# Optimization experiments

Hardware: AMD Instinct MI355X
Metric: run time of the kernel (lower is better)

Reference implementation:

```python
import jax, jax.numpy as jnp
import numpy as np

KNN = 32

def _sqdist(src, dst):
    # src [B,N,C], dst [B,M,C] -> [B,N,M]
    return (jnp.sum(src * src, -1)[:, :, None]
            + jnp.sum(dst * dst, -1)[:, None, :]
            - 2.0 * jnp.einsum('bnc,bmc->bnm', src, dst))

def _knn(points, queries, k):
    d = _sqdist(queries, points)
    neg_d, idx = jax.lax.top_k(-d, k)  # smallest-k, sorted ascending
    return -neg_d, idx

def _gather(points, idx):
    # points [B,N,C], idx [B,S,K] -> [B,S,K,C]
    return jax.vmap(lambda p, i: p[i])(points, idx)

def _bn(x, gamma, beta):
    # BatchNorm1d over channel dim, stats over (B, N), training-mode (biased var)
    mean = jnp.mean(x, axis=(0, 1), keepdims=True)
    var = jnp.var(x, axis=(0, 1), keepdims=True)
    return gamma * (x - mean) * jax.lax.rsqrt(var + 1e-5) + beta

def _lin_bn_act(x, W, b, gamma, beta):
    return jax.nn.leaky_relu(_bn(x @ W + b, gamma, beta), 0.2)

def _local_trans(feat, idx, qW, qb, kW, kb, vW, vb, rW, rb, rg, rbe, fW, fb, fg, fbe):
    # xyz=False, FPS_idx=None, usetanh=False branch of LocalTrans
    residual = _lin_bn_act(feat, rW, rb, rg, rbe)          # conv_res (residual=True)
    q = (feat @ qW + qb)[:, :, None, :]                    # [B,N,1,C]
    k = _gather(feat @ kW + kb, idx)                       # [B,N,K,C]
    v = _gather(feat @ vW + vb, idx)                       # [B,N,K,C]
    energy = (q - k) / jnp.sqrt(jnp.float32(qW.shape[-1]))
    att = jax.nn.softmax(energy, axis=2)                   # softmax over K
    att = att - jnp.sum(att, axis=2, keepdims=True)        # offset subtraction
    ctx = jnp.max(att * v, axis=2)                         # max-pool over K -> [B,N,C]
    return residual + _lin_bn_act(ctx, fW, fb, fg, fbe)    # ffn


def setup_inputs() -> dict:
    key = jax.random.key(0)
    ks = jax.random.split(key, 12)
    B, N, Cin, Cout = 4, 2048, 128, 256
    r = lambda k, s: jax.random.normal(k, s, dtype=jnp.float32)
    return {
        'xyz': r(ks[0], (B, N, 3)),
        'base_xyz': r(ks[1], (B, N, 3)),
        'feature': r(ks[2], (B, N, Cin)),
        'qW': r(ks[3], (2, Cin, Cout)) * 0.05, 'qb': jnp.zeros((2, Cout), jnp.float32),
        'kW': r(ks[4], (2, Cin, Cout)) * 0.05, 'kb': jnp.zeros((2, Cout), jnp.float32),
        'vW': r(ks[5], (2, Cin, Cout)) * 0.05, 'vb': jnp.zeros((2, Cout), jnp.float32),
        'resW': r(ks[6], (2, Cin, Cout)) * 0.05, 'resb': jnp.zeros((2, Cout), jnp.float32),
        'res_gamma': jnp.ones((2, Cout), jnp.float32), 'res_beta': jnp.zeros((2, Cout), jnp.float32),
        'ffnW': r(ks[7], (2, Cout, Cout)) * 0.05, 'ffnb': jnp.zeros((2, Cout), jnp.float32),
        'ffn_gamma': jnp.ones((2, Cout), jnp.float32), 'ffn_beta': jnp.zeros((2, Cout), jnp.float32),
        'fcW': r(ks[8], (2 * Cout, Cout)) * 0.05, 'fcb': jnp.zeros((Cout,), jnp.float32),
        'fc_gamma': jnp.ones((Cout,), jnp.float32), 'fc_beta': jnp.zeros((Cout,), jnp.float32),
    }


def reference(xyz, base_xyz, feature, qW, qb, kW, kb, vW, vb, resW, resb,
              res_gamma, res_beta, ffnW, ffnb, ffn_gamma, ffn_beta,
              fcW, fcb, fc_gamma, fc_beta):
    # LocalMerge.forward, branch: feature is not None, FPS_idx is None
    dist, idx = _knn(base_xyz, xyz, KNN)
    _, idx_feature = _knn(feature, feature, KNN)
    idxs = (idx, idx_feature)
    ms = [_local_trans(feature, idxs[i], qW[i], qb[i], kW[i], kb[i], vW[i], vb[i],
                       resW[i], resb[i], res_gamma[i], res_beta[i],
                       ffnW[i], ffnb[i], ffn_gamma[i], ffn_beta[i]) for i in range(2)]
    merge = _lin_bn_act(jnp.concatenate(ms, axis=2), fcW, fcb, fc_gamma, fc_beta)
    return merge
```

## Files before the change

kernel.cpp:

```cpp
#include <hip/hip_runtime.h>
#include <hip/hip_bf16.h>

typedef __hip_bfloat16 bf16;
typedef __attribute__((ext_vector_type(8))) short short8;
typedef __attribute__((ext_vector_type(4))) float f32x4;

#define ROWS 8192
#define NPTS 2048
#define CIN  128
#define COUT 256
#define KNN  32
#define PAD  132

__device__ inline float lrelu(float x){ return x >= 0.f ? x : 0.2f*x; }
__device__ inline unsigned short f2bf(float x){
  bf16 h = __float2bfloat16(x);
  return *(unsigned short*)&h;
}
__device__ inline float bf2f(unsigned short u){ return __uint_as_float((unsigned)u << 16); }
__device__ inline void stc(float* p, float v){ *p = v; }
__device__ inline void stc(unsigned short* p, float v){ *p = f2bf(v); }

#define N_WTX   (2048*CIN)
#define N_WFFN  (2*COUT*COUT)
#define N_WFC   (COUT*512)
#define N_FEAT  (ROWS*CIN)
__global__ __launch_bounds__(256) void pack_all(
    const float* qW, const float* kW, const float* vW, const float* rW,
    const float* qb, const float* kb, const float* vb, const float* rb,
    const float* ffnW, const float* fcW, const float* feature,
    unsigned short* WT_x, float* bcat, unsigned short* WT_ffn,
    unsigned short* WT_fc, unsigned short* feat_bf){
  int t = blockIdx.x*256 + threadIdx.x;
  if (t < N_WTX){
    int c = t >> 7, r = t & 127;
    int g = c >> 8, i = g >> 2, tt = g & 3, cc = c & 255;
    const float* W = (tt==0?qW: tt==1?kW: tt==2?vW: rW) + (size_t)i*CIN*COUT;
    WT_x[t] = f2bf(W[r*COUT + cc]);
    if (r == 0){
      const float* bb = (tt==0?qb: tt==1?kb: tt==2?vb: rb) + i*COUT;
      bcat[c] = bb[cc];
    }
  } else if (t < N_WTX + N_WFFN){
    int u = t - N_WTX;
    int i = u >> 16, n = (u >> 8) & 255, k = u & 255;
    WT_ffn[u] = f2bf(ffnW[(size_t)i*65536 + k*256 + n]);
  } else if (t < N_WTX + N_WFFN + N_WFC){
    int u = t - N_WTX - N_WFFN;
    int n = u >> 9, k = u & 511;
    WT_fc[u] = f2bf(fcW[(size_t)k*256 + n]);
  } else {
    int u = t - N_WTX - N_WFFN - N_WFC;
    feat_bf[u] = f2bf(feature[u]);
  }
}

__device__ inline unsigned dxf(float d){
  unsigned u = __float_as_uint(d);
  return (u & 0x80000000u) ? ~u : (u | 0x80000000u);
}
__device__ inline unsigned umin32(unsigned a, unsigned b){ return a < b ? a : b; }

#define DPP_ROW_SHR1    0x111
#define DPP_ROW_SHR2    0x112
#define DPP_ROW_SHR4    0x114
#define DPP_ROW_SHR8    0x118

template<int CTRL>
__device__ inline unsigned dpp_umin_step(unsigned v){
  unsigned s = (unsigned)__builtin_amdgcn_update_dpp((int)v, (int)v, CTRL, 0xF, 0xF, false);
  return s < v ? s : v;
}

#define TOPK32_CASE(G)                                                   \
  {                                                                      \
    int jw = 7;                                                          \
    _Pragma("unroll")                                                    \
    for (int j = 7; j >= 0; --j) if (k[G*8+j] == minv) jw = j;           \
    slot = G*8 + jw;                                                     \
    _Pragma("unroll")                                                    \
    for (int j = 0; j < 8; ++j) if (j == jw) k[G*8+j] = ~0u;             \
    unsigned nm = k[G*8];                                                \
    _Pragma("unroll")                                                    \
    for (int j = 1; j < 8; ++j) nm = umin32(nm, k[G*8+j]);               \
    g[G] = nm;                                                           \
  }

__device__ inline void wave_topk32_u32(unsigned* k, int lane, int* out){
  unsigned g[4];
  #pragma unroll
  for (int gi = 0; gi < 4; ++gi){
    unsigned m = k[gi*8];
    #pragma unroll
    for (int j = 1; j < 8; ++j) m = umin32(m, k[gi*8+j]);
    g[gi] = m;
  }
  unsigned outv = 0;
  for (int r = 0; r < KNN; ++r){
    unsigned lm = umin32(umin32(g[0], g[1]), umin32(g[2], g[3]));
    unsigned m = lm;
    m = dpp_umin_step<DPP_ROW_SHR1>(m);
    m = dpp_umin_step<DPP_ROW_SHR2>(m);
    m = dpp_umin_step<DPP_ROW_SHR4>(m);
    m = dpp_umin_step<DPP_ROW_SHR8>(m);
    unsigned b0 = (unsigned)__builtin_amdgcn_readlane((int)m, 15);
    unsigned b1 = (unsigned)__builtin_amdgcn_readlane((int)m, 31);
    unsigned b2 = (unsigned)__builtin_amdgcn_readlane((int)m, 47);
    unsigned b3 = (unsigned)__builtin_amdgcn_readlane((int)m, 63);
    unsigned minv = umin32(umin32(b0, b1), umin32(b2, b3));
    unsigned long long ball = __ballot(lm == minv);
    int owner = (int)__builtin_ctzll(ball);
    int slot = 0;
    if (owner == lane){
      int gw = (g[0]==minv) ? 0 : (g[1]==minv) ? 1 : (g[2]==minv) ? 2 : 3;
      if      (gw == 0) TOPK32_CASE(0)
      else if (gw == 1) TOPK32_CASE(1)
      else if (gw == 2) TOPK32_CASE(2)
      else              TOPK32_CASE(3)
    }
    int slotw = __builtin_amdgcn_readlane(slot, owner);
    unsigned wm = (unsigned)(owner*32 + slotw);
    outv = (lane == r) ? wm : outv;
  }
  if (lane < KNN) out[lane] = (int)outv;
}

__device__ inline unsigned dkey_xyz(float qq, float q0, float q1, float q2,
                                    float p0, float p1, float p2){
  float pp = __fadd_rn(__fadd_rn(__fmul_rn(p0,p0), __fmul_rn(p1,p1)), __fmul_rn(p2,p2));
  float dot = __fmul_rn(q0,p0);
  dot = __fadd_rn(dot, __fmul_rn(q1,p1));
  dot = __fadd_rn(dot, __fmul_rn(q2,p2));
  float d = __fsub_rn(__fadd_rn(qq, pp), __fmul_rn(2.f, dot));
  return dxf(d);
}

__global__ __launch_bounds__(256, 6) void knn_xyz_kernel(const float* xyz, const float* base, int* idx_out){
  int wave = threadIdx.x >> 6;
  int lane = threadIdx.x & 63;
  int bid = blockIdx.x*4 + wave;
  int b = bid >> 11;
  float q0 = xyz[(size_t)bid*3+0];
  float q1 = xyz[(size_t)bid*3+1];
  float q2 = xyz[(size_t)bid*3+2];
  float qq = __fadd_rn(__fadd_rn(__fmul_rn(q0,q0), __fmul_rn(q1,q1)), __fmul_rn(q2,q2));
  const float4* p4 = (const float4*)(base + (size_t)b*NPTS*3 + (size_t)lane*96);
  unsigned k[32];
  #pragma unroll
  for (int c = 0; c < 8; ++c){
    float4 f0 = p4[c*3+0];
    float4 f1 = p4[c*3+1];
    float4 f2 = p4[c*3+2];
    k[c*4+0] = dkey_xyz(qq,q0,q1,q2, f0.x, f0.y, f0.z);
    k[c*4+1] = dkey_xyz(qq,q0,q1,q2, f0.w, f1.x, f1.y);
    k[c*4+2] = dkey_xyz(qq,q0,q1,q2, f1.z, f1.w, f2.x);
    k[c*4+3] = dkey_xyz(qq,q0,q1,q2, f2.y, f2.z, f2.w);
  }
  wave_topk32_u32(k, lane, idx_out + (size_t)bid*KNN);
}

__global__ __launch_bounds__(256) void rownorm_kernel(const float* feat, float* nrm){
  int row = blockIdx.x*256 + threadIdx.x;
  const float* f = feat + (size_t)row*CIN;
  float L[16];
  #pragma unroll
  for (int l = 0; l < 16; ++l){
    float x0 = __fmul_rn(f[l],     f[l]);
    float x1 = __fmul_rn(f[16+l],  f[16+l]);
    float x2 = __fmul_rn(f[32+l],  f[32+l]);
    float x3 = __fmul_rn(f[48+l],  f[48+l]);
    float x4 = __fmul_rn(f[64+l],  f[64+l]);
    float x5 = __fmul_rn(f[80+l],  f[80+l]);
    float x6 = __fmul_rn(f[96+l],  f[96+l]);
    float x7 = __fmul_rn(f[112+l], f[112+l]);
    L[l] = __fadd_rn(
        __fadd_rn(__fadd_rn(x0,x1), __fadd_rn(x2,x3)),
        __fadd_rn(__fadd_rn(x4,x5), __fadd_rn(x6,x7)));
  }
  float T2[4];
  #pragma unroll
  for (int i = 0; i < 4; ++i)
    T2[i] = __fadd_rn(__fadd_rn(L[i], L[i+8]), __fadd_rn(L[i+4], L[i+12]));
  nrm[row] = __fadd_rn(__fadd_rn(T2[0], T2[2]), __fadd_rn(T2[1], T2[3]));
}

__global__ __launch_bounds__(256) void dist_feat_kernel(const float* fb, const float* nrm, float* D){
  __shared__ float Aq[32*PAD];
  __shared__ float Bm[32*PAD];
  int nb = blockIdx.y*32, mb = blockIdx.x*32;
  int t = threadIdx.x;
  {
    int r = t >> 3, c16 = (t & 7) << 4;
    const float* an = fb + (size_t)(nb + r)*CIN + c16;
    const float* bm = fb + (size_t)(mb + r)*CIN + c16;
    #pragma unroll
    for (int j = 0; j < 4; ++j){
      *(float4*)&Aq[r*PAD + c16 + 4*j] = *(const float4*)&an[4*j];
      *(float4*)&Bm[r*PAD + c16 + 4*j] = *(const float4*)&bm[4*j];
    }
  }
  __syncthreads();
  int tx = t & 15, ty = t >> 4;
  const float* qa0 = &Aq[(ty     )*PAD];
  const float* qa1 = &Aq[(ty + 16)*PAD];
  const float* ma0 = &Bm[(tx     )*PAD];
  const float* ma1 = &Bm[(tx + 16)*PAD];
  float P[2][2][16];
  #pragma unroll
  for (int l = 0; l < 16; ++l){
    float a0 = qa0[48+l], a1 = qa1[48+l], b0 = ma0[48+l], b1 = ma1[48+l];
    P[0][0][l] = __fmul_rn(a0,b0); P[0][1][l] = __fmul_rn(a0,b1);
    P[1][0][l] = __fmul_rn(a1,b0); P[1][1][l] = __fmul_rn(a1,b1);
  }
  const int segs[7] = {32,16,0,112,96,80,64};
  #pragma unroll
  for (int s = 0; s < 7; ++s){
    int off = segs[s];
    #pragma unroll
    for (int l = 0; l < 16; ++l){
      float a0 = qa0[off+l], a1 = qa1[off+l], b0 = ma0[off+l], b1 = ma1[off+l];
      P[0][0][l] = __fmaf_rn(a0,b0,P[0][0][l]); P[0][1][l] = __fmaf_rn(a0,b1,P[0][1][l]);
      P[1][0][l] = __fmaf_rn(a1,b0,P[1][0][l]); P[1][1][l] = __fmaf_rn(a1,b1,P[1][1][l]);
    }
  }
  #pragma unroll
  for (int i = 0; i < 2; ++i){
    int n = nb + ty + 16*i;
    float nn = nrm[n];
    #pragma unroll
    for (int j = 0; j < 2; ++j){
      float T2[4];
      #pragma unroll
      for (int q = 0; q < 4; ++q)
        T2[q] = __fadd_rn(__fadd_rn(P[i][j][q], P[i][j][q+8]), __fadd_rn(P[i][j][q+4], P[i][j][q+12]));
      float dot = __fadd_rn(__fadd_rn(T2[0], T2[2]), __fadd_rn(T2[1], T2[3]));
      int m = mb + tx + 16*j;
      D[(size_t)n*NPTS + m] = __fsub_rn(__fadd_rn(nn, nrm[m]), __fmul_rn(2.f, dot));
    }
  }
}

__global__ __launch_bounds__(256, 6) void topk_row_kernel(const float* D, int* idx_out){
  int wave = threadIdx.x >> 6;
  int lane = threadIdx.x & 63;
  int n = blockIdx.x*4 + wave;
  const float* src = D + (size_t)n*NPTS + lane*32;
  unsigned k[32];
  #pragma unroll
  for (int i = 0; i < 8; ++i){
    float4 v = *(const float4*)&src[i*4];
    k[i*4+0] = dxf(v.x);
    k[i*4+1] = dxf(v.y);
    k[i*4+2] = dxf(v.z);
    k[i*4+3] = dxf(v.w);
  }
  wave_topk32_u32(k, lane, idx_out + (size_t)n*KNN);
}

template<typename CT>
__global__ __launch_bounds__(256) void mfma_gemm(const unsigned short* __restrict__ A,
                                                 const unsigned short* __restrict__ Bt,
                                                 const float* __restrict__ bias,
                                                 CT* __restrict__ C, int N, int K,
                                                 size_t sA, size_t sB, size_t sBias, size_t sC){
  int z = blockIdx.z;
  A += (size_t)z*sA; Bt += (size_t)z*sB; bias += (size_t)z*sBias; C += (size_t)z*sC;
  __shared__ unsigned short As[64*40];
  __shared__ unsigned short Bs[64*40];
  int nb = blockIdx.x*64, mb = blockIdx.y*64;
  int t = threadIdx.x;
  int wave = t >> 6, lane = t & 63;
  int m16 = lane & 15, quad = lane >> 4;
  f32x4 acc[4];
  #pragma unroll
  for (int s = 0; s < 4; ++s) acc[s] = (f32x4){0.f, 0.f, 0.f, 0.f};
  int srow = t >> 2, skseg = (t & 3) << 3;
  for (int kt = 0; kt < K; kt += 32){
    __syncthreads();
    *(uint4*)&As[srow*40 + skseg] = *(const uint4*)&A [(size_t)(mb + srow)*K + kt + skseg];
    *(uint4*)&Bs[srow*40 + skseg] = *(const uint4*)&Bt[(size_t)(nb + srow)*K + kt + skseg];
    __syncthreads();
    short8 a = *(const short8*)&As[(wave*16 + m16)*40 + quad*8];
    #pragma unroll
    for (int s = 0; s < 4; ++s){
      short8 b = *(const short8*)&Bs[(s*16 + m16)*40 + quad*8];
      acc[s] = __builtin_amdgcn_mfma_f32_16x16x32_bf16(a, b, acc[s], 0, 0, 0);
    }
  }
  #pragma unroll
  for (int s = 0; s < 4; ++s){
    int col = nb + s*16 + m16;
    float bv = bias[col];
    #pragma unroll
    for (int r = 0; r < 4; ++r){
      int row = mb + wave*16 + quad*4 + r;
      stc(&C[(size_t)row*N + col], acc[s][r] + bv);
    }
  }
}

__global__ __launch_bounds__(256) void attn_kernel(const unsigned short* X,
                                                   const int* idx0, const int* idx1,
                                                   unsigned short* ctx){
  int i = blockIdx.y;
  const int* ip = (i == 0 ? idx0 : idx1);
  int local = threadIdx.x & 127;
  int r     = threadIdx.x >> 7;
  int bn    = blockIdx.x*2 + r;
  int b     = bn >> 11;
  __shared__ int jr[2][KNN];
  if (local < KNN) jr[r][local] = (b << 11) + ip[(size_t)bn*KNN + local];
  __syncthreads();
  const ushort2* X2 = (const ushort2*)X;
  size_t boff = (size_t)i*512 + local;
  ushort2 q2 = X2[(size_t)bn*1024 + boff];
  float qx = bf2f(q2.x), qy = bf2f(q2.y);
  float ex[KNN], ey[KNN];
  float mx = -3.4e38f, my = -3.4e38f;
  #pragma unroll
  for (int k = 0; k < KNN; ++k){
    ushort2 k2 = X2[(size_t)jr[r][k]*1024 + boff + 128];
    ex[k] = (qx - bf2f(k2.x)) * 0.0625f;
    ey[k] = (qy - bf2f(k2.y)) * 0.0625f;
    mx = fmaxf(mx, ex[k]);
    my = fmaxf(my, ey[k]);
  }
  float sx = 0.f, sy = 0.f;
  #pragma unroll
  for (int k = 0; k < KNN; ++k){
    sx += __expf(ex[k] - mx);
    sy += __expf(ey[k] - my);
  }
  float ix = 1.f / sx, iy = 1.f / sy;
  float bx = -3.4e38f, by = -3.4e38f;
  #pragma unroll
  for (int k = 0; k < KNN; ++k){
    ushort2 v2 = X2[(size_t)jr[r][k]*1024 + boff + 256];
    float ax = __expf(ex[k] - mx)*ix - 1.0f;
    float ay = __expf(ey[k] - my)*iy - 1.0f;
    bx = fmaxf(bx, ax*bf2f(v2.x));
    by = fmaxf(by, ay*bf2f(v2.y));
  }
  ushort2 o; o.x = f2bf(bx); o.y = f2bf(by);
  ((ushort2*)ctx)[((size_t)i*ROWS + bn)*128 + local] = o;
}

__global__ __launch_bounds__(256) void bnx_partial(const unsigned short* X, float* partial){
  int p = blockIdx.x, i = blockIdx.y, c = threadIdx.x;
  const unsigned short* base = X + (size_t)i*1024 + 768 + c;
  float s = 0.f, s2 = 0.f;
  for (int r = 0; r < 256; ++r){
    float v = bf2f(base[(size_t)(p*256 + r)*2048]);
    s += v; s2 += v*v;
  }
  partial[((size_t)i*32 + p)*512 + c]       = s;
  partial[((size_t)i*32 + p)*512 + 256 + c] = s2;
}

__global__ __launch_bounds__(256) void bnf_partial(const unsigned short* F, float* partial){
  int p = blockIdx.x, i = blockIdx.y, c = threadIdx.x;
  const unsigned short* base = F + (size_t)i*ROWS*COUT + c;
  float s = 0.f, s2 = 0.f;
  for (int r = 0; r < 256; ++r){
    float v = bf2f(base[(size_t)(p*256 + r)*COUT]);
    s += v; s2 += v*v;
  }
  partial[((size_t)i*32 + p)*512 + c]       = s;
  partial[((size_t)i*32 + p)*512 + 256 + c] = s2;
}

__global__ __launch_bounds__(256) void bny_partial(const float* Y, float* partial){
  int p = blockIdx.x, c = threadIdx.x;
  float s = 0.f, s2 = 0.f;
  for (int r = 0; r < 256; ++r){
    float v = Y[(size_t)(p*256 + r)*COUT + c];
    s += v; s2 += v*v;
  }
  partial[p*512 + c]       = s;
  partial[p*512 + 256 + c] = s2;
}

__global__ __launch_bounds__(256) void bn_final2(const float* partial, float* stats){
  int i = blockIdx.y, c = threadIdx.x;
  partial += (size_t)i*32*512;
  stats   += (size_t)i*512;
  float s = 0.f, s2 = 0.f;
  for (int p = 0; p < 32; ++p){ s += partial[p*512 + c]; s2 += partial[p*512 + 256 + c]; }
  float mean = s * (1.f/8192.f);
  float var  = s2 * (1.f/8192.f) - mean*mean;
  stats[c]       = mean;
  stats[256 + c] = 1.f / sqrtf(var + 1e-5f);
}

__global__ __launch_bounds__(256) void build_m_kernel(const unsigned short* X, const unsigned short* F,
    const float* stats, const float* gR, const float* bR, const float* gF, const float* bF,
    unsigned short* M){
  int bn = blockIdx.x, c = threadIdx.x;
  #pragma unroll
  for (int i = 0; i < 2; ++i){
    float r  = bf2f(X[(size_t)bn*2048 + i*1024 + 768 + c]);
    float rv = gR[i*COUT+c] * (r - stats[i*512+c]) * stats[i*512+256+c] + bR[i*COUT+c];
    rv = lrelu(rv);
    float f  = bf2f(F[(size_t)i*ROWS*COUT + (size_t)bn*COUT + c]);
    float fv = gF[i*COUT+c] * (f - stats[(2+i)*512+c]) * stats[(2+i)*512+256+c] + bF[i*COUT+c];
    fv = lrelu(fv);
    M[(size_t)bn*512 + i*COUT + c] = f2bf(rv + fv);
  }
}

__global__ __launch_bounds__(256) void final_kernel(const float* Y, const float* stats,
                                                    const float* g, const float* be, float* out){
  int bn = blockIdx.x, c = threadIdx.x;
  float y = Y[(size_t)bn*COUT + c];
  float v = g[c] * (y - stats[c]) * stats[256+c] + be[c];
  out[(size_t)bn*COUT + c] = lrelu(v);
}

extern "C" void kernel_launch(void* const* d_in, const int* in_sizes, int n_in,
                              void* d_out, int out_size, void* d_ws, size_t ws_size,
                              hipStream_t stream){
  const float* xyz      = (const float*)d_in[0];
  const float* base_xyz = (const float*)d_in[1];
  const float* feature  = (const float*)d_in[2];
  const float* qW = (const float*)d_in[3];
  const float* qb = (const float*)d_in[4];
  const float* kW = (const float*)d_in[5];
  const float* kb = (const float*)d_in[6];
  const float* vW = (const float*)d_in[7];
  const float* vb = (const float*)d_in[8];
  const float* rW = (const float*)d_in[9];
  const float* rb = (const float*)d_in[10];
  const float* res_gamma = (const float*)d_in[11];
  const float* res_beta  = (const float*)d_in[12];
  const float* ffnW = (const float*)d_in[13];
  const float* ffnb = (const float*)d_in[14];
  const float* ffn_gamma = (const float*)d_in[15];
  const float* ffn_beta  = (const float*)d_in[16];
  const float* fcW = (const float*)d_in[17];
  const float* fcb = (const float*)d_in[18];
  const float* fc_gamma = (const float*)d_in[19];
  const float* fc_beta  = (const float*)d_in[20];
  float* out = (float*)d_out;

  char* ws = (char*)d_ws;
  size_t o = 0;
  auto alloc = [&](size_t bytes)->char*{
    char* p = ws + o;
    o += (bytes + 255) & ~(size_t)255;
    return p;
  };
  int*            idx0    = (int*)           alloc((size_t)ROWS*KNN*4);
  int*            idx1    = (int*)           alloc((size_t)ROWS*KNN*4);
  float*          nrm     = (float*)         alloc((size_t)ROWS*4);
  float*          bcat    = (float*)         alloc((size_t)2048*4);
  unsigned short* WT_x    = (unsigned short*)alloc((size_t)2048*CIN*2);
  unsigned short* WT_ffn  = (unsigned short*)alloc((size_t)2*COUT*COUT*2);
  unsigned short* WT_fc   = (unsigned short*)alloc((size_t)COUT*512*2);
  unsigned short* feat_bf = (unsigned short*)alloc((size_t)ROWS*CIN*2);
  float*          stats   = (float*)         alloc((size_t)5*512*4);
  float*          partial = (float*)         alloc((size_t)2*32*512*4);
  char*           R1      = alloc((size_t)ROWS*2048*2);
  char*           R2      = alloc((size_t)ROWS*COUT*4);
  unsigned short* Mmat_bf = (unsigned short*)alloc((size_t)ROWS*512*2);
  unsigned short* F_bf    = (unsigned short*)alloc((size_t)2*ROWS*COUT*2);
  float*          Dbuf = (float*)R1;
  unsigned short* X_bf = (unsigned short*)R1;
  unsigned short* ctx_bf = (unsigned short*)R2;
  float*          Y    = (float*)R2;

  pack_all<<<(N_WTX+N_WFFN+N_WFC+N_FEAT)/256, 256, 0, stream>>>(
      qW,kW,vW,rW,qb,kb,vb,rb, ffnW, fcW, feature, WT_x, bcat, WT_ffn, WT_fc, feat_bf);

  knn_xyz_kernel<<<ROWS/4, 256, 0, stream>>>(xyz, base_xyz, idx0);
  rownorm_kernel<<<ROWS/256, 256, 0, stream>>>(feature, nrm);

  for (int b = 0; b < 4; ++b){
    const float* fb = feature + (size_t)b*NPTS*CIN;
    dist_feat_kernel<<<dim3(NPTS/32, NPTS/32), 256, 0, stream>>>(
        fb, nrm + (size_t)b*NPTS, Dbuf);
    topk_row_kernel<<<NPTS/4, 256, 0, stream>>>(Dbuf, idx1 + (size_t)b*NPTS*KNN);
  }

  mfma_gemm<unsigned short><<<dim3(2048/64, ROWS/64, 1), 256, 0, stream>>>(
      feat_bf, WT_x, bcat, X_bf, 2048, CIN, 0, 0, 0, 0);

  attn_kernel<<<dim3(ROWS/2, 2), 256, 0, stream>>>(X_bf, idx0, idx1, ctx_bf);

  bnx_partial<<<dim3(32, 2), 256, 0, stream>>>(X_bf, partial);
  bn_final2<<<dim3(1, 2), 256, 0, stream>>>(partial, stats);

  mfma_gemm<unsigned short><<<dim3(COUT/64, ROWS/64, 2), 256, 0, stream>>>(
      ctx_bf, WT_ffn, ffnb, F_bf, COUT, COUT,
      (size_t)ROWS*COUT, (size_t)COUT*COUT, COUT, (size_t)ROWS*COUT);

  bnf_partial<<<dim3(32, 2), 256, 0, stream>>>(F_bf, partial);
  bn_final2<<<dim3(1, 2), 256, 0, stream>>>(partial, stats + 2*512);

  build_m_kernel<<<ROWS, 256, 0, stream>>>(X_bf, F_bf, stats,
      res_gamma, res_beta, ffn_gamma, ffn_beta, Mmat_bf);

  mfma_gemm<float><<<dim3(COUT/64, ROWS/64, 1), 256, 0, stream>>>(
      Mmat_bf, WT_fc, fcb, Y, COUT, 512, 0, 0, 0, 0);

  bny_partial<<<32, 256, 0, stream>>>(Y, partial);
  bn_final2<<<dim3(1, 1), 256, 0, stream>>>(partial, stats + 4*512);

  final_kernel<<<ROWS, 256, 0, stream>>>(Y, stats + 4*512, fc_gamma, fc_beta, out);
}
```

Baseline: 471.8 us.

## Exploit distance symmetry, precompute base point norms, cache softmax exponentials

The feature self-distance kernel now computes only the upper-triangular tiles and writes each tile's transpose through shared memory, roughly halving the FMA work. The base_xyz squared norms are precomputed once in the packing kernel instead of being recomputed by every query wave in the xyz kNN. The attention kernel keeps its exponentials in registers instead of computing them twice. The risks are higher register pressure in attention, an extra shared-memory transpose pass, and uneven block work in the distance kernel.

```diff
diff --git a/kernel.cpp b/kernel.cpp
--- a/kernel.cpp
+++ b/kernel.cpp
@@ -25,12 +25,13 @@
 #define N_WFFN  (2*COUT*COUT)
 #define N_WFC   (COUT*512)
 #define N_FEAT  (ROWS*CIN)
+#define N_PP    8192
 __global__ __launch_bounds__(256) void pack_all(
     const float* qW, const float* kW, const float* vW, const float* rW,
     const float* qb, const float* kb, const float* vb, const float* rb,
-    const float* ffnW, const float* fcW, const float* feature,
+    const float* ffnW, const float* fcW, const float* feature, const float* base_xyz,
     unsigned short* WT_x, float* bcat, unsigned short* WT_ffn,
-    unsigned short* WT_fc, unsigned short* feat_bf){
+    unsigned short* WT_fc, unsigned short* feat_bf, float* ppxyz){
   int t = blockIdx.x*256 + threadIdx.x;
   if (t < N_WTX){
     int c = t >> 7, r = t & 127;
@@ -49,9 +50,15 @@
     int u = t - N_WTX - N_WFFN;
     int n = u >> 9, k = u & 511;
     WT_fc[u] = f2bf(fcW[(size_t)k*256 + n]);
-  } else {
+  } else if (t < N_WTX + N_WFFN + N_WFC + N_FEAT){
     int u = t - N_WTX - N_WFFN - N_WFC;
     feat_bf[u] = f2bf(feature[u]);
+  } else {
+    int u = t - N_WTX - N_WFFN - N_WFC - N_FEAT;
+    float p0 = base_xyz[(size_t)u*3+0];
+    float p1 = base_xyz[(size_t)u*3+1];
+    float p2 = base_xyz[(size_t)u*3+2];
+    ppxyz[u] = __fadd_rn(__fadd_rn(__fmul_rn(p0,p0), __fmul_rn(p1,p1)), __fmul_rn(p2,p2));
   }
 }
 
@@ -126,8 +133,7 @@
 }
 
 __device__ inline unsigned dkey_xyz(float qq, float q0, float q1, float q2,
-                                    float p0, float p1, float p2){
-  float pp = __fadd_rn(__fadd_rn(__fmul_rn(p0,p0), __fmul_rn(p1,p1)), __fmul_rn(p2,p2));
+                                    float p0, float p1, float p2, float pp){
   float dot = __fmul_rn(q0,p0);
   dot = __fadd_rn(dot, __fmul_rn(q1,p1));
   dot = __fadd_rn(dot, __fmul_rn(q2,p2));
@@ -135,7 +141,8 @@
   return dxf(d);
 }
 
-__global__ __launch_bounds__(256, 6) void knn_xyz_kernel(const float* xyz, const float* base, int* idx_out){
+__global__ __launch_bounds__(256, 6) void knn_xyz_kernel(const float* xyz, const float* base,
+                                                         const float* ppxyz, int* idx_out){
   int wave = threadIdx.x >> 6;
   int lane = threadIdx.x & 63;
   int bid = blockIdx.x*4 + wave;
@@ -145,16 +152,18 @@
   float q2 = xyz[(size_t)bid*3+2];
   float qq = __fadd_rn(__fadd_rn(__fmul_rn(q0,q0), __fmul_rn(q1,q1)), __fmul_rn(q2,q2));
   const float4* p4 = (const float4*)(base + (size_t)b*NPTS*3 + (size_t)lane*96);
+  const float4* n4 = (const float4*)(ppxyz + (size_t)b*NPTS + (size_t)lane*32);
   unsigned k[32];
   #pragma unroll
   for (int c = 0; c < 8; ++c){
     float4 f0 = p4[c*3+0];
     float4 f1 = p4[c*3+1];
     float4 f2 = p4[c*3+2];
-    k[c*4+0] = dkey_xyz(qq,q0,q1,q2, f0.x, f0.y, f0.z);
-    k[c*4+1] = dkey_xyz(qq,q0,q1,q2, f0.w, f1.x, f1.y);
-    k[c*4+2] = dkey_xyz(qq,q0,q1,q2, f1.z, f1.w, f2.x);
-    k[c*4+3] = dkey_xyz(qq,q0,q1,q2, f2.y, f2.z, f2.w);
+    float4 pn = n4[c];
+    k[c*4+0] = dkey_xyz(qq,q0,q1,q2, f0.x, f0.y, f0.z, pn.x);
+    k[c*4+1] = dkey_xyz(qq,q0,q1,q2, f0.w, f1.x, f1.y, pn.y);
+    k[c*4+2] = dkey_xyz(qq,q0,q1,q2, f1.z, f1.w, f2.x, pn.z);
+    k[c*4+3] = dkey_xyz(qq,q0,q1,q2, f2.y, f2.z, f2.w, pn.w);
   }
   wave_topk32_u32(k, lane, idx_out + (size_t)bid*KNN);
 }
@@ -188,6 +197,7 @@
   __shared__ float Aq[32*PAD];
   __shared__ float Bm[32*PAD];
   int nb = blockIdx.y*32, mb = blockIdx.x*32;
+  if (mb < nb) return;
   int t = threadIdx.x;
   {
     int r = t >> 3, c16 = (t & 7) << 4;
@@ -223,6 +233,7 @@
       P[1][0][l] = __fmaf_rn(a1,b0,P[1][0][l]); P[1][1][l] = __fmaf_rn(a1,b1,P[1][1][l]);
     }
   }
+  float val[2][2];
   #pragma unroll
   for (int i = 0; i < 2; ++i){
     int n = nb + ty + 16*i;
@@ -235,9 +246,24 @@
         T2[q] = __fadd_rn(__fadd_rn(P[i][j][q], P[i][j][q+8]), __fadd_rn(P[i][j][q+4], P[i][j][q+12]));
       float dot = __fadd_rn(__fadd_rn(T2[0], T2[2]), __fadd_rn(T2[1], T2[3]));
       int m = mb + tx + 16*j;
-      D[(size_t)n*NPTS + m] = __fsub_rn(__fadd_rn(nn, nrm[m]), __fmul_rn(2.f, dot));
-    }
-  }
+      float v = __fsub_rn(__fadd_rn(nn, nrm[m]), __fmul_rn(2.f, dot));
+      val[i][j] = v;
+      D[(size_t)n*NPTS + m] = v;
+    }
+  }
+  __syncthreads();
+  float* Tt = Aq;
+  #pragma unroll
+  for (int i = 0; i < 2; ++i)
+    #pragma unroll
+    for (int j = 0; j < 2; ++j)
+      Tt[(tx + 16*j)*33 + (ty + 16*i)] = val[i][j];
+  __syncthreads();
+  #pragma unroll
+  for (int i = 0; i < 2; ++i)
+    #pragma unroll
+    for (int j = 0; j < 2; ++j)
+      D[(size_t)(mb + ty + 16*i)*NPTS + (nb + tx + 16*j)] = Tt[(ty + 16*i)*33 + (tx + 16*j)];
 }
 
 __global__ __launch_bounds__(256, 6) void topk_row_kernel(const float* D, int* idx_out){
@@ -328,16 +354,18 @@
   float sx = 0.f, sy = 0.f;
   #pragma unroll
   for (int k = 0; k < KNN; ++k){
-    sx += __expf(ex[k] - mx);
-    sy += __expf(ey[k] - my);
+    ex[k] = __expf(ex[k] - mx);
+    ey[k] = __expf(ey[k] - my);
+    sx += ex[k];
+    sy += ey[k];
   }
   float ix = 1.f / sx, iy = 1.f / sy;
   float bx = -3.4e38f, by = -3.4e38f;
   #pragma unroll
   for (int k = 0; k < KNN; ++k){
     ushort2 v2 = X2[(size_t)jr[r][k]*1024 + boff + 256];
-    float ax = __expf(ex[k] - mx)*ix - 1.0f;
-    float ay = __expf(ey[k] - my)*iy - 1.0f;
+    float ax = ex[k]*ix - 1.0f;
+    float ay = ey[k]*iy - 1.0f;
     bx = fmaxf(bx, ax*bf2f(v2.x));
     by = fmaxf(by, ay*bf2f(v2.y));
   }
@@ -452,6 +480,7 @@
   int*            idx0    = (int*)           alloc((size_t)ROWS*KNN*4);
   int*            idx1    = (int*)           alloc((size_t)ROWS*KNN*4);
   float*          nrm     = (float*)         alloc((size_t)ROWS*4);
+  float*          ppxyz   = (float*)         alloc((size_t)N_PP*4);
   float*          bcat    = (float*)         alloc((size_t)2048*4);
   unsigned short* WT_x    = (unsigned short*)alloc((size_t)2048*CIN*2);
   unsigned short* WT_ffn  = (unsigned short*)alloc((size_t)2*COUT*COUT*2);
@@ -468,10 +497,11 @@
   unsigned short* ctx_bf = (unsigned short*)R2;
   float*          Y    = (float*)R2;
 
-  pack_all<<<(N_WTX+N_WFFN+N_WFC+N_FEAT)/256, 256, 0, stream>>>(
-      qW,kW,vW,rW,qb,kb,vb,rb, ffnW, fcW, feature, WT_x, bcat, WT_ffn, WT_fc, feat_bf);
-
-  knn_xyz_kernel<<<ROWS/4, 256, 0, stream>>>(xyz, base_xyz, idx0);
+  pack_all<<<(N_WTX+N_WFFN+N_WFC+N_FEAT+N_PP)/256, 256, 0, stream>>>(
+      qW,kW,vW,rW,qb,kb,vb,rb, ffnW, fcW, feature, base_xyz,
+      WT_x, bcat, WT_ffn, WT_fc, feat_bf, ppxyz);
+
+  knn_xyz_kernel<<<ROWS/4, 256, 0, stream>>>(xyz, base_xyz, ppxyz, idx0);
   rownorm_kernel<<<ROWS/256, 256, 0, stream>>>(feature, nrm);
 
   for (int b = 0; b < 4; ++b){
```

Result: faster. 448.5 us (-4.9%).
